# Kernel optimization log

Measured on AMD Instinct MI355X. Metric: run time of the kernel, lower is better.

## Reference

```python
import jax, jax.numpy as jnp
import numpy as np

N_NODES, D_NODE = 100000, 128
N_EDGES, D_EDGE = 1000000, 32
D_IN = 2 * D_NODE + D_EDGE  # 288
H1, H2, D_OUT = 128, 64, 1


def setup_inputs() -> dict:
    key = jax.random.key(0)
    ks = jax.random.split(key, 9)
    x = jax.random.normal(ks[0], (N_NODES, D_NODE), dtype=jnp.float32)
    edge_index = jax.random.randint(ks[1], (2, N_EDGES), 0, N_NODES, dtype=jnp.int64)
    edge_features = jax.random.normal(ks[2], (N_EDGES, D_EDGE), dtype=jnp.float32)
    def lin(kw, kb, fan_in, fan_out):
        bound = 1.0 / np.sqrt(fan_in)
        W = jax.random.uniform(kw, (fan_in, fan_out), minval=-bound, maxval=bound, dtype=jnp.float32)
        b = jax.random.uniform(kb, (fan_out,), minval=-bound, maxval=bound, dtype=jnp.float32)
        return W, b
    W1, b1 = lin(ks[3], ks[4], D_IN, H1)
    W2, b2 = lin(ks[5], ks[6], H1, H2)
    W3, b3 = lin(ks[7], ks[8], H2, D_OUT)
    return {"x": x, "edge_index": edge_index, "edge_features": edge_features,
            "W1": W1, "b1": b1, "W2": W2, "b2": b2, "W3": W3, "b3": b3}


def reference(x, edge_index, edge_features, W1, b1, W2, b2, W3, b3):
    origin, destination = edge_index[0], edge_index[1]
    # [E, 2*D_NODE + D_EDGE]
    z = jnp.concatenate([x[origin], x[destination], edge_features], axis=1)
    z = jax.nn.leaky_relu(z @ W1 + b1)  # negative_slope=0.01, matches torch default
    z = jax.nn.leaky_relu(z @ W2 + b2)
    z = z @ W3 + b3
    return z.reshape(-1)
```

## Files before the change

kernel.cpp:

```cpp
#include <hip/hip_runtime.h>

#define N_NODES 100000
#define N_EDGES 1000000

typedef __attribute__((ext_vector_type(8))) short bf16x8;
typedef __attribute__((ext_vector_type(4))) float f32x4;
typedef __attribute__((ext_vector_type(4))) unsigned u32x4;

static __device__ __forceinline__ short f2bf(float f) {
    unsigned u = __float_as_uint(f);
    u = (u + 0x7fffu + ((u >> 16) & 1u)) >> 16;
    return (short)u;
}
static __device__ __forceinline__ float bf2f(unsigned short s) {
    return __uint_as_float(((unsigned)s) << 16);
}
static __device__ __forceinline__ float lrelu(float x) {
    return fmaxf(x, 0.01f * x);
}
static __device__ __forceinline__ unsigned cvtpk(float lo, float hi) {
    unsigned r;
    asm("v_cvt_pk_bf16_f32 %0, %1, %2" : "=v"(r) : "v"(lo), "v"(hi));
    return r;
}

__global__ __launch_bounds__(256) void precompute_mfma(
    const float* __restrict__ x, const float* __restrict__ W1,
    const float* __restrict__ b1, unsigned short* __restrict__ Pb,
    unsigned short* __restrict__ Qb)
{
    const int t    = threadIdx.x;
    const int lane = t & 63;
    const int w    = t >> 6;
    const int q    = lane >> 4;
    const int n15  = lane & 15;
    const int chb  = 64 * w;

    bf16x8 afrag[4][4];
    #pragma unroll
    for (int mtl = 0; mtl < 4; ++mtl) {
        const int ch = chb + 16 * mtl + n15;
        const float* wcol = (ch < 128) ? (W1 + ch) : (W1 + 128 * 128 + (ch - 128));
        #pragma unroll
        for (int ks = 0; ks < 4; ++ks)
            #pragma unroll
            for (int j = 0; j < 8; ++j)
                afrag[mtl][ks][j] = f2bf(wcol[(size_t)(32 * ks + 8 * q + j) * 128]);
    }
    float b1r[16];
    #pragma unroll
    for (int mtl = 0; mtl < 4; ++mtl)
        #pragma unroll
        for (int r = 0; r < 4; ++r) {
            const int ch = chb + 16 * mtl + 4 * q + r;
            b1r[mtl * 4 + r] = (ch < 128) ? b1[ch] : 0.0f;
        }

    unsigned short* tbase = (w < 2) ? Pb : Qb;
    const int mtb = 4 * (w & 1);

    for (int tile = blockIdx.x; tile < N_NODES / 16; tile += gridDim.x) {
        const int n0 = tile * 16;
        const float* xrow = x + (size_t)(n0 + n15) * 128;

        bf16x8 bfr[4];
        #pragma unroll
        for (int ks = 0; ks < 4; ++ks) {
            f32x4 xa = *(const f32x4*)(xrow + 32 * ks + 8 * q);
            f32x4 xb = *(const f32x4*)(xrow + 32 * ks + 8 * q + 4);
            u32x4 bu;
            bu[0] = cvtpk(xa[0], xa[1]);
            bu[1] = cvtpk(xa[2], xa[3]);
            bu[2] = cvtpk(xb[0], xb[1]);
            bu[3] = cvtpk(xb[2], xb[3]);
            bfr[ks] = __builtin_bit_cast(bf16x8, bu);
        }
        #pragma unroll
        for (int mtl = 0; mtl < 4; ++mtl) {
            f32x4 acc = {0.f, 0.f, 0.f, 0.f};
            #pragma unroll
            for (int ks = 0; ks < 4; ++ks)
                acc = __builtin_amdgcn_mfma_f32_16x16x32_bf16(afrag[mtl][ks], bfr[ks], acc, 0, 0, 0);
            unsigned* dst = (unsigned*)(tbase + (size_t)(n0 + n15) * 128 + q * 32 + (mtb + mtl) * 4);
            dst[0] = cvtpk(acc[0] + b1r[mtl * 4 + 0], acc[1] + b1r[mtl * 4 + 1]);
            dst[1] = cvtpk(acc[2] + b1r[mtl * 4 + 2], acc[3] + b1r[mtl * 4 + 3]);
        }
    }
}

__global__ __launch_bounds__(256, 3) void edge_mfma(
    const int* __restrict__ ei, const float* __restrict__ ef,
    const float* __restrict__ W1, const float* __restrict__ W2,
    const float* __restrict__ b2, const float* __restrict__ W3,
    const float* __restrict__ b3, const unsigned short* __restrict__ Pb,
    const unsigned short* __restrict__ Qb, float* __restrict__ out)
{
    __shared__ unsigned short w2s[16 * 64 * 8];
    __shared__ unsigned short a1s[8 * 64 * 8];
    const int t    = threadIdx.x;
    const int lane = t & 63;
    const int w    = t >> 6;
    const int q    = lane >> 4;
    const int n15  = lane & 15;

    #pragma unroll
    for (int i = 0; i < 2; ++i) {
        const int mt = 2 * w + i;
        bf16x8 f;
        #pragma unroll
        for (int j = 0; j < 8; ++j)
            f[j] = f2bf(W1[(size_t)(256 + 8 * q + j) * 128 + 16 * mt + n15]);
        *(bf16x8*)&a1s[(mt * 64 + lane) * 8] = f;
    }

    {
        const int mt2 = w;
        #pragma unroll
        for (int ks = 0; ks < 4; ++ks) {
            bf16x8 f;
            #pragma unroll
            for (int j = 0; j < 8; ++j) {
                const int ch = 32 * ks + ((j < 4) ? (4 * q + j) : (16 + 4 * q + (j - 4)));
                f[j] = f2bf(W2[(size_t)ch * 64 + 16 * mt2 + n15]);
            }
            *(bf16x8*)&w2s[(((mt2 << 2) | ks) * 64 + lane) * 8] = f;
        }
    }

    unsigned b2w3[16];
    #pragma unroll
    for (int mt2 = 0; mt2 < 4; ++mt2)
        #pragma unroll
        for (int r = 0; r < 4; ++r) {
            const int ch = 16 * mt2 + 4 * q + r;
            b2w3[mt2 * 4 + r] = (unsigned)(unsigned short)f2bf(b2[ch])
                              | ((unsigned)(unsigned short)f2bf(W3[ch]) << 16);
        }
    const float b3v = b3[0];

    __syncthreads();

    const int nTiles  = N_EDGES / 16;
    const int wid     = blockIdx.x * 4 + w;
    const int wstride = gridDim.x * 4;
    if (wid >= nTiles) return;

    int tile0 = wid;
    int tile1 = tile0 + wstride;
    bool have1 = tile1 < nTiles;

    int oi0, di0; f32x4 ea0, eb0;
    {
        const int e0 = tile0 * 16;
        oi0 = ei[e0 + n15];
        di0 = ei[N_EDGES + e0 + n15];
        ea0 = *(const f32x4*)(ef + (size_t)(e0 + n15) * 32 + 8 * q);
        eb0 = *(const f32x4*)(ef + (size_t)(e0 + n15) * 32 + 8 * q + 4);
    }
    int oi1 = 0, di1 = 0; f32x4 ea1 = ea0, eb1 = eb0;
    if (have1) {
        const int e1 = tile1 * 16;
        oi1 = ei[e1 + n15];
        di1 = ei[N_EDGES + e1 + n15];
        ea1 = *(const f32x4*)(ef + (size_t)(e1 + n15) * 32 + 8 * q);
        eb1 = *(const f32x4*)(ef + (size_t)(e1 + n15) * 32 + 8 * q + 4);
    }
    bf16x8 pvb[4], qvb[4];
    {
        const unsigned short* prow = Pb + (size_t)oi0 * 128 + q * 32;
        const unsigned short* qrow = Qb + (size_t)di0 * 128 + q * 32;
        #pragma unroll
        for (int c = 0; c < 4; ++c) {
            pvb[c] = *(const bf16x8*)(prow + 8 * c);
            qvb[c] = *(const bf16x8*)(qrow + 8 * c);
        }
    }

    while (true) {
        u32x4 befu;
        befu[0] = cvtpk(ea0[0], ea0[1]);
        befu[1] = cvtpk(ea0[2], ea0[3]);
        befu[2] = cvtpk(eb0[0], eb0[1]);
        befu[3] = cvtpk(eb0[2], eb0[3]);
        const bf16x8 bef = __builtin_bit_cast(bf16x8, befu);

        const int  tile2 = tile1 + wstride;
        const bool have2 = have1 && (tile2 < nTiles);
        int oi2 = oi1, di2 = di1; f32x4 ea2 = ea1, eb2 = eb1;
        if (have2) {
            const int e2 = tile2 * 16;
            oi2 = ei[e2 + n15];
            ndi2:
            di2 = ei[N_EDGES + e2 + n15];
            ea2 = *(const f32x4*)(ef + (size_t)(e2 + n15) * 32 + 8 * q);
            eb2 = *(const f32x4*)(ef + (size_t)(e2 + n15) * 32 + 8 * q + 4);
        }

        u32x4 hfu[4];
        #pragma unroll
        for (int mt = 0; mt < 8; ++mt) {
            const bf16x8 a1f = *(const bf16x8*)&a1s[(mt * 64 + lane) * 8];
            f32x4 z = {0.f, 0.f, 0.f, 0.f};
            f32x4 h = __builtin_amdgcn_mfma_f32_16x16x32_bf16(a1f, bef, z, 0, 0, 0);
            const int c = mt >> 1, off = (mt & 1) * 4;
            float v0 = lrelu(h[0] + bf2f((unsigned short)pvb[c][off + 0]) + bf2f((unsigned short)qvb[c][off + 0]));
            float v1 = lrelu(h[1] + bf2f((unsigned short)pvb[c][off + 1]) + bf2f((unsigned short)qvb[c][off + 1]));
            float v2 = lrelu(h[2] + bf2f((unsigned short)pvb[c][off + 2]) + bf2f((unsigned short)qvb[c][off + 2]));
            float v3 = lrelu(h[3] + bf2f((unsigned short)pvb[c][off + 3]) + bf2f((unsigned short)qvb[c][off + 3]));
            hfu[mt >> 1][(mt & 1) * 2 + 0] = cvtpk(v0, v1);
            hfu[mt >> 1][(mt & 1) * 2 + 1] = cvtpk(v2, v3);
        }

        if (have1) {
            const unsigned short* prow = Pb + (size_t)oi1 * 128 + q * 32;
            const unsigned short* qrow = Qb + (size_t)di1 * 128 + q * 32;
            #pragma unroll
            for (int c = 0; c < 4; ++c) {
                pvb[c] = *(const bf16x8*)(prow + 8 * c);
                qvb[c] = *(const bf16x8*)(qrow + 8 * c);
            }
        }

        f32x4 acc2[4] = {{0.f,0.f,0.f,0.f},{0.f,0.f,0.f,0.f},{0.f,0.f,0.f,0.f},{0.f,0.f,0.f,0.f}};
        #pragma unroll
        for (int ks = 0; ks < 4; ++ks) {
            const bf16x8 hfrag = __builtin_bit_cast(bf16x8, hfu[ks]);
            #pragma unroll
            for (int mt2 = 0; mt2 < 4; ++mt2) {
                const bf16x8 a2f = *(const bf16x8*)&w2s[(((mt2 << 2) | ks) * 64 + lane) * 8];
                acc2[mt2] = __builtin_amdgcn_mfma_f32_16x16x32_bf16(a2f, hfrag, acc2[mt2], 0, 0, 0);
            }
        }

        float s = 0.0f;
        #pragma unroll
        for (int mt2 = 0; mt2 < 4; ++mt2)
            #pragma unroll
            for (int r = 0; r < 4; ++r) {
                const unsigned u = b2w3[mt2 * 4 + r];
                float v = acc2[mt2][r] + bf2f((unsigned short)(u & 0xffffu));
                v = lrelu(v);
                s += v * __uint_as_float(u & 0xffff0000u);
            }
        s += __shfl_xor(s, 16);
        s += __shfl_xor(s, 32);
        if (q == 0) out[tile0 * 16 + n15] = s + b3v;

        if (!have1) break;
        tile0 = tile1; tile1 = tile2; have1 = have2;
        oi1 = oi2; di1 = di2;
        ea0 = ea1; eb0 = eb1; ea1 = ea2; eb1 = eb2;
    }
}

extern "C" void kernel_launch(void* const* d_in, const int* in_sizes, int n_in,
                              void* d_out, int out_size, void* d_ws, size_t ws_size,
                              hipStream_t stream) {
    const float* x   = (const float*)d_in[0];
    const int*   ei  = (const int*)d_in[1];
    const float* ef  = (const float*)d_in[2];
    const float* W1  = (const float*)d_in[3];
    const float* b1  = (const float*)d_in[4];
    const float* W2  = (const float*)d_in[5];
    const float* b2  = (const float*)d_in[6];
    const float* W3  = (const float*)d_in[7];
    const float* b3  = (const float*)d_in[8];
    float*       out = (float*)d_out;

    unsigned short* Pb = (unsigned short*)d_ws;
    unsigned short* Qb = Pb + (size_t)N_NODES * 128;

    precompute_mfma<<<2048, 256, 0, stream>>>(x, W1, b1, Pb, Qb);
    edge_mfma<<<768, 256, 0, stream>>>(ei, ef, W1, W2, b2, W3, b3, Pb, Qb, out);
}
```

Baseline: 351.5 us.

## Deepen gather prefetch pipeline with double-buffered P/Q rows

Restructures the persistent edge-tile loop so that P/Q row gathers are issued two tiles ahead into alternating A/B register buffers, with index and edge-feature loads three tiles ahead. The loop is unrolled by two via a macro so the buffers swap statically. This is meant to hide more of the random-gather latency behind the MFMA work, at the cost of extra VGPRs and possibly lower occupancy.

```diff
diff --git a/kernel.cpp b/kernel.cpp
--- a/kernel.cpp
+++ b/kernel.cpp
@@ -145,112 +145,141 @@
     const int wstride = gridDim.x * 4;
     if (wid >= nTiles) return;
 
-    int tile0 = wid;
-    int tile1 = tile0 + wstride;
-    bool have1 = tile1 < nTiles;
-
-    int oi0, di0; f32x4 ea0, eb0;
+    int t0 = wid, t1 = t0 + wstride, t2 = t1 + wstride;
+    bool h1 = t1 < nTiles, h2 = t2 < nTiles;
+
+    int oi0, di0, oi1, di1, oi2, di2;
+    f32x4 ea0, eb0, ea1, eb1, ea2, eb2;
     {
-        const int e0 = tile0 * 16;
+        const int e0 = t0 * 16;
         oi0 = ei[e0 + n15];
         di0 = ei[N_EDGES + e0 + n15];
         ea0 = *(const f32x4*)(ef + (size_t)(e0 + n15) * 32 + 8 * q);
         eb0 = *(const f32x4*)(ef + (size_t)(e0 + n15) * 32 + 8 * q + 4);
     }
-    int oi1 = 0, di1 = 0; f32x4 ea1 = ea0, eb1 = eb0;
-    if (have1) {
-        const int e1 = tile1 * 16;
+    oi1 = oi0; di1 = di0; ea1 = ea0; eb1 = eb0;
+    if (h1) {
+        const int e1 = t1 * 16;
         oi1 = ei[e1 + n15];
         di1 = ei[N_EDGES + e1 + n15];
         ea1 = *(const f32x4*)(ef + (size_t)(e1 + n15) * 32 + 8 * q);
         eb1 = *(const f32x4*)(ef + (size_t)(e1 + n15) * 32 + 8 * q + 4);
     }
-    bf16x8 pvb[4], qvb[4];
+    oi2 = oi1; di2 = di1; ea2 = ea1; eb2 = eb1;
+    if (h2) {
+        const int e2 = t2 * 16;
+        oi2 = ei[e2 + n15];
+        di2 = ei[N_EDGES + e2 + n15];
+        ea2 = *(const f32x4*)(ef + (size_t)(e2 + n15) * 32 + 8 * q);
+        eb2 = *(const f32x4*)(ef + (size_t)(e2 + n15) * 32 + 8 * q + 4);
+    }
+
+    bf16x8 pvbA[4], qvbA[4], pvbB[4], qvbB[4];
     {
         const unsigned short* prow = Pb + (size_t)oi0 * 128 + q * 32;
         const unsigned short* qrow = Qb + (size_t)di0 * 128 + q * 32;
         #pragma unroll
         for (int c = 0; c < 4; ++c) {
-            pvb[c] = *(const bf16x8*)(prow + 8 * c);
-            qvb[c] = *(const bf16x8*)(qrow + 8 * c);
-        }
-    }
-
-    while (true) {
-        u32x4 befu;
-        befu[0] = cvtpk(ea0[0], ea0[1]);
-        befu[1] = cvtpk(ea0[2], ea0[3]);
-        befu[2] = cvtpk(eb0[0], eb0[1]);
-        befu[3] = cvtpk(eb0[2], eb0[3]);
-        const bf16x8 bef = __builtin_bit_cast(bf16x8, befu);
-
-        const int  tile2 = tile1 + wstride;
-        const bool have2 = have1 && (tile2 < nTiles);
-        int oi2 = oi1, di2 = di1; f32x4 ea2 = ea1, eb2 = eb1;
-        if (have2) {
-            const int e2 = tile2 * 16;
-            oi2 = ei[e2 + n15];
-            ndi2:
-            di2 = ei[N_EDGES + e2 + n15];
-            ea2 = *(const f32x4*)(ef + (size_t)(e2 + n15) * 32 + 8 * q);
-            eb2 = *(const f32x4*)(ef + (size_t)(e2 + n15) * 32 + 8 * q + 4);
-        }
-
-        u32x4 hfu[4];
-        #pragma unroll
-        for (int mt = 0; mt < 8; ++mt) {
-            const bf16x8 a1f = *(const bf16x8*)&a1s[(mt * 64 + lane) * 8];
-            f32x4 z = {0.f, 0.f, 0.f, 0.f};
-            f32x4 h = __builtin_amdgcn_mfma_f32_16x16x32_bf16(a1f, bef, z, 0, 0, 0);
-            const int c = mt >> 1, off = (mt & 1) * 4;
-            float v0 = lrelu(h[0] + bf2f((unsigned short)pvb[c][off + 0]) + bf2f((unsigned short)qvb[c][off + 0]));
-            float v1 = lrelu(h[1] + bf2f((unsigned short)pvb[c][off + 1]) + bf2f((unsigned short)qvb[c][off + 1]));
-            float v2 = lrelu(h[2] + bf2f((unsigned short)pvb[c][off + 2]) + bf2f((unsigned short)qvb[c][off + 2]));
-            float v3 = lrelu(h[3] + bf2f((unsigned short)pvb[c][off + 3]) + bf2f((unsigned short)qvb[c][off + 3]));
-            hfu[mt >> 1][(mt & 1) * 2 + 0] = cvtpk(v0, v1);
-            hfu[mt >> 1][(mt & 1) * 2 + 1] = cvtpk(v2, v3);
-        }
-
-        if (have1) {
-            const unsigned short* prow = Pb + (size_t)oi1 * 128 + q * 32;
-            const unsigned short* qrow = Qb + (size_t)di1 * 128 + q * 32;
-            #pragma unroll
-            for (int c = 0; c < 4; ++c) {
-                pvb[c] = *(const bf16x8*)(prow + 8 * c);
-                qvb[c] = *(const bf16x8*)(qrow + 8 * c);
-            }
-        }
-
-        f32x4 acc2[4] = {{0.f,0.f,0.f,0.f},{0.f,0.f,0.f,0.f},{0.f,0.f,0.f,0.f},{0.f,0.f,0.f,0.f}};
-        #pragma unroll
-        for (int ks = 0; ks < 4; ++ks) {
-            const bf16x8 hfrag = __builtin_bit_cast(bf16x8, hfu[ks]);
-            #pragma unroll
-            for (int mt2 = 0; mt2 < 4; ++mt2) {
-                const bf16x8 a2f = *(const bf16x8*)&w2s[(((mt2 << 2) | ks) * 64 + lane) * 8];
-                acc2[mt2] = __builtin_amdgcn_mfma_f32_16x16x32_bf16(a2f, hfrag, acc2[mt2], 0, 0, 0);
-            }
-        }
-
-        float s = 0.0f;
-        #pragma unroll
-        for (int mt2 = 0; mt2 < 4; ++mt2)
-            #pragma unroll
-            for (int r = 0; r < 4; ++r) {
-                const unsigned u = b2w3[mt2 * 4 + r];
-                float v = acc2[mt2][r] + bf2f((unsigned short)(u & 0xffffu));
-                v = lrelu(v);
-                s += v * __uint_as_float(u & 0xffff0000u);
-            }
-        s += __shfl_xor(s, 16);
-        s += __shfl_xor(s, 32);
-        if (q == 0) out[tile0 * 16 + n15] = s + b3v;
-
-        if (!have1) break;
-        tile0 = tile1; tile1 = tile2; have1 = have2;
-        oi1 = oi2; di1 = di2;
-        ea0 = ea1; eb0 = eb1; ea1 = ea2; eb1 = eb2;
-    }
+            pvbA[c] = *(const bf16x8*)(prow + 8 * c);
+            qvbA[c] = *(const bf16x8*)(qrow + 8 * c);
+        }
+    }
+    if (h1) {
+        const unsigned short* prow = Pb + (size_t)oi1 * 128 + q * 32;
+        const unsigned short* qrow = Qb + (size_t)di1 * 128 + q * 32;
+        #pragma unroll
+        for (int c = 0; c < 4; ++c) {
+            pvbB[c] = *(const bf16x8*)(prow + 8 * c);
+            qvbB[c] = *(const bf16x8*)(qrow + 8 * c);
+        }
+    } else {
+        #pragma unroll
+        for (int c = 0; c < 4; ++c) { pvbB[c] = pvbA[c]; qvbB[c] = qvbA[c]; }
+    }
+
+#define STEP(PC, QC)                                                           \
+    {                                                                          \
+        u32x4 befu;                                                            \
+        befu[0] = cvtpk(ea0[0], ea0[1]);                                       \
+        befu[1] = cvtpk(ea0[2], ea0[3]);                                       \
+        befu[2] = cvtpk(eb0[0], eb0[1]);                                       \
+        befu[3] = cvtpk(eb0[2], eb0[3]);                                       \
+        const bf16x8 bef = __builtin_bit_cast(bf16x8, befu);                   \
+        const int  t3 = t2 + wstride;                                          \
+        const bool h3 = h2 && (t3 < nTiles);                                   \
+        int oi3 = oi2, di3 = di2;                                              \
+        f32x4 ea3 = ea2, eb3 = eb2;                                            \
+        if (h3) {                                                              \
+            const int e3 = t3 * 16;                                            \
+            oi3 = ei[e3 + n15];                                                \
+            di3 = ei[N_EDGES + e3 + n15];                                      \
+            ea3 = *(const f32x4*)(ef + (size_t)(e3 + n15) * 32 + 8 * q);       \
+            eb3 = *(const f32x4*)(ef + (size_t)(e3 + n15) * 32 + 8 * q + 4);   \
+        }                                                                      \
+        \
+        u32x4 hfu[4];                                                          \
+        _Pragma("unroll")                                                      \
+        for (int mt = 0; mt < 8; ++mt) {                                       \
+            const bf16x8 a1f = *(const bf16x8*)&a1s[(mt * 64 + lane) * 8];     \
+            f32x4 z = {0.f, 0.f, 0.f, 0.f};                                    \
+            f32x4 hh = __builtin_amdgcn_mfma_f32_16x16x32_bf16(a1f, bef, z, 0, 0, 0); \
+            const int c = mt >> 1, off = (mt & 1) * 4;                         \
+            float v0 = lrelu(hh[0] + bf2f((unsigned short)PC[c][off + 0]) + bf2f((unsigned short)QC[c][off + 0])); \
+            float v1 = lrelu(hh[1] + bf2f((unsigned short)PC[c][off + 1]) + bf2f((unsigned short)QC[c][off + 1])); \
+            float v2 = lrelu(hh[2] + bf2f((unsigned short)PC[c][off + 2]) + bf2f((unsigned short)QC[c][off + 2])); \
+            float v3 = lrelu(hh[3] + bf2f((unsigned short)PC[c][off + 3]) + bf2f((unsigned short)QC[c][off + 3])); \
+            hfu[mt >> 1][(mt & 1) * 2 + 0] = cvtpk(v0, v1);                    \
+            hfu[mt >> 1][(mt & 1) * 2 + 1] = cvtpk(v2, v3);                    \
+        }                                                                      \
+        \
+        \
+        if (h2) {                                                              \
+            const unsigned short* prow = Pb + (size_t)oi2 * 128 + q * 32;      \
+            const unsigned short* qrow = Qb + (size_t)di2 * 128 + q * 32;      \
+            _Pragma("unroll")                                                  \
+            for (int c2 = 0; c2 < 4; ++c2) {                                   \
+                PC[c2] = *(const bf16x8*)(prow + 8 * c2);                      \
+                QC[c2] = *(const bf16x8*)(qrow + 8 * c2);                      \
+            }                                                                  \
+        }                                                                      \
+                  \
+        f32x4 acc2[4] = {{0.f,0.f,0.f,0.f},{0.f,0.f,0.f,0.f},{0.f,0.f,0.f,0.f},{0.f,0.f,0.f,0.f}}; \
+        _Pragma("unroll")                                                      \
+        for (int ks = 0; ks < 4; ++ks) {                                       \
+            const bf16x8 hfrag = __builtin_bit_cast(bf16x8, hfu[ks]);          \
+            _Pragma("unroll")                                                  \
+            for (int mt2 = 0; mt2 < 4; ++mt2) {                                \
+                const bf16x8 a2f = *(const bf16x8*)&w2s[(((mt2 << 2) | ks) * 64 + lane) * 8]; \
+                acc2[mt2] = __builtin_amdgcn_mfma_f32_16x16x32_bf16(a2f, hfrag, acc2[mt2], 0, 0, 0); \
+            }                                                                  \
+        }                                                                      \
+                          \
+        float s = 0.0f;                                                        \
+        _Pragma("unroll")                                                      \
+        for (int mt2 = 0; mt2 < 4; ++mt2)                                      \
+            _Pragma("unroll")                                                  \
+            for (int r = 0; r < 4; ++r) {                                      \
+                const unsigned u = b2w3[mt2 * 4 + r];                          \
+                float v = acc2[mt2][r] + bf2f((unsigned short)(u & 0xffffu));  \
+                v = lrelu(v);                                                  \
+                s += v * __uint_as_float(u & 0xffff0000u);                     \
+            }                                                                  \
+        s += __shfl_xor(s, 16);                                                \
+        s += __shfl_xor(s, 32);                                                \
+        if (q == 0) out[t0 * 16 + n15] = s + b3v;                              \
+        if (!h1) goto done;                                                    \
+        t0 = t1; t1 = t2; t2 = t3;                                             \
+        h1 = h2; h2 = h3;                                                      \
+        ea0 = ea1; eb0 = eb1; ea1 = ea2; eb1 = eb2; ea2 = ea3; eb2 = eb3;      \
+        oi2 = oi3; di2 = di3;                                                  \
+    }
+
+    for (;;) {
+        STEP(pvbA, qvbA);
+        STEP(pvbB, qvbB);
+    }
+done: ;
+#undef STEP
 }
 
 extern "C" void kernel_launch(void* const* d_in, const int* in_sizes, int n_in,
```

New measurement: 356.6 us. About the same (+1.4%).
